# Performance work log

Hardware: AMD Instinct MI355X
Metric: run time of the kernel (lower is better)

## Reference

```python
import jax, jax.numpy as jnp
import numpy as np


def setup_inputs() -> dict:
    key = jax.random.key(0)
    ks = jax.random.split(key, 6)
    B, S, I, H = 8, 4096, 512, 512
    scale = 1.0 / np.sqrt(I)
    return {
        "x": jax.random.normal(ks[0], (B, S, I), dtype=jnp.float32),
        "h_0": jax.random.normal(ks[1], (B, H), dtype=jnp.float32),
        "W_z": jax.random.normal(ks[2], (H, I), dtype=jnp.float32) * scale,
        "b_z": jax.random.normal(ks[3], (H,), dtype=jnp.float32) * scale,
        "W_h": jax.random.normal(ks[4], (H, I), dtype=jnp.float32) * scale,
        "b_h": jax.random.normal(ks[5], (H,), dtype=jnp.float32) * scale,
    }


def reference(x, h_0, W_z, b_z, W_h, b_h):
    # Gate and candidate projections (dense GEMMs over all timesteps at once)
    z = jax.nn.sigmoid(jnp.einsum("bsi,hi->bsh", x, W_z) + b_z)  # [B,S,H]
    h_tilde = jnp.einsum("bsi,hi->bsh", x, W_h) + b_h            # [B,S,H]

    # Linear recurrence h_t = a_t * h_{t-1} + b_t with a = 1-z, b = z*h_tilde.
    # Parallel associative scan over time; h_0 folded in as element 0 (a=1, b=h_0).
    a = jnp.concatenate([jnp.ones_like(h_0)[:, None, :], 1.0 - z], axis=1)     # [B,S+1,H]
    b = jnp.concatenate([h_0[:, None, :], z * h_tilde], axis=1)                # [B,S+1,H]

    def combine(c1, c2):
        a1, b1 = c1
        a2, b2 = c2
        return a1 * a2, a2 * b1 + b2

    _, h = jax.lax.associative_scan(combine, (a, b), axis=1)
    return h[:, 1:, :]  # drop the h_0 slot -> [B,S,H]
```

## Files before the change

### kernel.cpp

```cpp
#include <hip/hip_runtime.h>
#include <hip/hip_bf16.h>
#include <stdint.h>


typedef __attribute__((ext_vector_type(8))) short short8;
typedef __attribute__((ext_vector_type(4))) float f32x4;

#define AS1 __attribute__((address_space(1)))
#define AS3 __attribute__((address_space(3)))

__device__ inline void gload_lds16(const void* g, void* l) {
  __builtin_amdgcn_global_load_lds((AS1 uint32_t*)(g), (AS3 uint32_t*)(l), 16, 0, 0);
}

__device__ inline ushort f2bf(float f) {
  union { __hip_bfloat16 h; ushort u; } v;
  v.h = __float2bfloat16(f);
  return v.u;
}

__global__ void cvt_all(const float* __restrict__ x,
                        const float* __restrict__ wz,
                        const float* __restrict__ wh,
                        ushort* __restrict__ xb,
                        ushort* __restrict__ wzb,
                        ushort* __restrict__ whb) {
  int i = blockIdx.x * 256 + threadIdx.x;
  for (; i < 4325376; i += 2048 * 256) {
    const float* s; ushort* d; int j;
    if (i < 4194304)      { s = x;  d = xb;  j = i; }
    else if (i < 4259840) { s = wz; d = wzb; j = i - 4194304; }
    else                  { s = wh; d = whb; j = i - 4259840; }
    float4 v = reinterpret_cast<const float4*>(s)[j];
    ushort4 o = make_ushort4(f2bf(v.x), f2bf(v.y), f2bf(v.z), f2bf(v.w));
    reinterpret_cast<ushort4*>(d)[j] = o;
  }
}

__global__ __launch_bounds__(256) void gemm_gate(
    const ushort* __restrict__ xb,
    const ushort* __restrict__ wzb,
    const ushort* __restrict__ whb,
    const float* __restrict__ b_z,
    const float* __restrict__ b_h,
    uint* __restrict__ ab,
    float2* __restrict__ ABc)
{
  __shared__ __align__(16) char smem[65536];

  const int t  = threadIdx.x;
  const int w  = t >> 6;
  const int l  = t & 63;
  const int lm = l & 15;
  const int lk = l >> 4;
  const int wm = w >> 1, wn = w & 1;
  const int bx = blockIdx.x;
  const int m0 = bx * 128;
  const int n0 = blockIdx.y * 64;

  const int srow = t >> 2;
  const int ssl  = t & 3;

  f32x4 accz[4][2], acch[4][2];
  #pragma unroll
  for (int m = 0; m < 4; ++m)
    #pragma unroll
    for (int n = 0; n < 2; ++n) {
      accz[m][n] = (f32x4){0.f, 0.f, 0.f, 0.f};
      acch[m][n] = (f32x4){0.f, 0.f, 0.f, 0.f};
    }

  auto stage = [&](int sel, int kt) {
    char* base = smem + sel * 16384;
    const int k0 = kt * 32;
    #pragma unroll
    for (int j = 0; j < 2; ++j) {
      int row = j * 64 + srow;
      int gs  = ssl ^ ((row >> 1) & 3);
      gload_lds16(xb + (size_t)(m0 + row) * 512 + k0 + gs * 8,
                  base + j * 4096 + w * 1024);
    }
    {
      int row = srow;
      int gs  = ssl ^ ((row >> 1) & 3);
      gload_lds16(wzb + (size_t)(n0 + row) * 512 + k0 + gs * 8,
                  base + 8192 + w * 1024);
      gload_lds16(whb + (size_t)(n0 + row) * 512 + k0 + gs * 8,
                  base + 12288 + w * 1024);
    }
  };

  stage(0, 0);
  stage(1, 1);
  stage(2, 2);

  #pragma unroll
  for (int kt = 0; kt < 16; ++kt) {
    const int sel = kt & 3;
    if (kt < 13) {
      stage((kt + 3) & 3, kt + 3);
      asm volatile("s_waitcnt vmcnt(12)" ::: "memory");
    } else if (kt == 13) {
      asm volatile("s_waitcnt vmcnt(8)" ::: "memory");
    } else if (kt == 14) {
      asm volatile("s_waitcnt vmcnt(4)" ::: "memory");
    } else {
      asm volatile("s_waitcnt vmcnt(0)" ::: "memory");
    }
    __builtin_amdgcn_s_barrier();

    const char* base = smem + sel * 16384;
    short8 af[4], bfz[2], bfh[2];
    #pragma unroll
    for (int m = 0; m < 4; ++m) {
      int row = wm * 64 + m * 16 + lm;
      af[m] = *(const short8*)(base + row * 64 + ((lk ^ ((row >> 1) & 3)) << 4));
    }
    #pragma unroll
    for (int n = 0; n < 2; ++n) {
      int row = wn * 32 + n * 16 + lm;
      int so  = ((lk ^ ((row >> 1) & 3)) << 4);
      bfz[n] = *(const short8*)(base + 8192  + row * 64 + so);
      bfh[n] = *(const short8*)(base + 12288 + row * 64 + so);
    }
    __builtin_amdgcn_s_setprio(1);
    #pragma unroll
    for (int m = 0; m < 4; ++m)
      #pragma unroll
      for (int n = 0; n < 2; ++n) {
        accz[m][n] = __builtin_amdgcn_mfma_f32_16x16x32_bf16(af[m], bfz[n], accz[m][n], 0, 0, 0);
        acch[m][n] = __builtin_amdgcn_mfma_f32_16x16x32_bf16(af[m], bfh[n], acch[m][n], 0, 0, 0);
      }
    __builtin_amdgcn_s_setprio(0);
    __builtin_amdgcn_s_barrier();
  }

  float bzv[2], bhv[2];
  #pragma unroll
  for (int n = 0; n < 2; ++n) {
    int col = n0 + wn * 32 + n * 16 + lm;
    bzv[n] = b_z[col];
    bhv[n] = b_h[col];
  }

  float av[4][4][2], bv[4][4][2];
  #pragma unroll
  for (int m = 0; m < 4; ++m) {
    #pragma unroll
    for (int j = 0; j < 4; ++j) {
      size_t grow = (size_t)(m0 + wm * 64 + m * 16 + lk * 4 + j);
      uint* po = ab + grow * 512 + n0 + wn * 32 + lm;
      #pragma unroll
      for (int n = 0; n < 2; ++n) {
        float uz = accz[m][n][j] + bzv[n];
        float uh = acch[m][n][j] + bhv[n];
        float z  = 1.f / (1.f + __expf(-uz));
        float a  = 1.f - z;
        float bb = z * uh;
        av[m][j][n] = a;
        bv[m][j][n] = bb;
        po[n * 16] = (uint)f2bf(a) | ((uint)f2bf(bb) << 16);
      }
    }
  }

  #pragma unroll
  for (int cb = 0; cb < 2; ++cb) {
    #pragma unroll
    for (int n = 0; n < 2; ++n) {
      float At[2], Bt[2];
      #pragma unroll
      for (int mm = 0; mm < 2; ++mm) {
        float A = 1.f, Bv = 0.f;
        #pragma unroll
        for (int j = 0; j < 4; ++j) {
          float a = av[2 * cb + mm][j][n];
          float b = bv[2 * cb + mm][j][n];
          A  = a * A;
          Bv = a * Bv + b;
        }
        float Ag = 1.f, Bg = 0.f;
        #pragma unroll
        for (int q = 0; q < 4; ++q) {
          float Aq = __shfl(A,  lm + 16 * q);
          float Bq = __shfl(Bv, lm + 16 * q);
          Ag = Aq * Ag;
          Bg = Aq * Bg + Bq;
        }
        At[mm] = Ag;
        Bt[mm] = Bg;
      }
      float Achunk = At[1] * At[0];
      float Bchunk = At[1] * Bt[0] + Bt[1];
      if (lk == 0) {
        int bidx = bx >> 5;
        int c    = (bx & 31) * 4 + wm * 2 + cb;
        int col  = n0 + wn * 32 + n * 16 + lm;
        ABc[((size_t)bidx * 512 + col) * 128 + c] = make_float2(Achunk, Bchunk);
      }
    }
  }
}

__global__ __launch_bounds__(256) void chunk_scan(
    const float2* __restrict__ ABc,
    const float* __restrict__ h0,
    float* __restrict__ Hinit)
{
  __shared__ float sm[128][4];
  const int w = threadIdx.x >> 6, l = threadIdx.x & 63;
  const int b   = blockIdx.x >> 7;
  const int h0g = (blockIdx.x & 127) * 4;
  const int h   = h0g + w;

  const float2* base = ABc + ((size_t)b * 512 + h) * 128;
  float2 s1 = base[l];
  float2 s2 = base[64 + l];

  float A1 = s1.x, B1 = s1.y;
  #pragma unroll
  for (int d = 1; d < 64; d <<= 1) {
    float uA = __shfl_up(A1, d);
    float uB = __shfl_up(B1, d);
    if (l >= d) { B1 = A1 * uB + B1; A1 = A1 * uA; }
  }
  float A2 = s2.x, B2 = s2.y;
  #pragma unroll
  for (int d = 1; d < 64; d <<= 1) {
    float uA = __shfl_up(A2, d);
    float uB = __shfl_up(B2, d);
    if (l >= d) { B2 = A2 * uB + B2; A2 = A2 * uA; }
  }
  float PA = __shfl(A1, 63), PB = __shfl(B1, 63);
  float FA = A2 * PA;
  float FB = A2 * PB + B2;

  float e1A = __shfl_up(A1, 1), e1B = __shfl_up(B1, 1);
  if (l == 0) { e1A = 1.f; e1B = 0.f; }
  float e2A = __shfl_up(FA, 1), e2B = __shfl_up(FB, 1);
  if (l == 0) { e2A = PA; e2B = PB; }

  float h0v = h0[b * 512 + h];
  sm[l][w]      = e1A * h0v + e1B;
  sm[64 + l][w] = e2A * h0v + e2B;
  __syncthreads();

  const int tt = threadIdx.x;
  if (tt < 128) {
    float4 v = *(const float4*)sm[tt];
    *(float4*)(Hinit + ((size_t)b * 128 + tt) * 512 + h0g) = v;
  }
}

__global__ __launch_bounds__(256) void scan_write(
    const uint* __restrict__ ab,
    const float* __restrict__ Hinit,
    float* __restrict__ out)
{
  int tid = blockIdx.x * 256 + threadIdx.x;
  int cg = tid & 127;
  int c  = (tid >> 7) & 127;
  int b  = tid >> 14;
  const uint4* p = reinterpret_cast<const uint4*>(ab + ((size_t)(b * 4096 + c * 32)) * 512) + cg;
  float4 hv = *reinterpret_cast<const float4*>(Hinit + ((size_t)b * 128 + c) * 512 + cg * 4);
  float4* po = reinterpret_cast<float4*>(out + ((size_t)(b * 4096 + c * 32)) * 512) + cg;
  #pragma unroll 4
  for (int t = 0; t < 32; ++t) {
    uint4 u = p[(size_t)t * 128];
    hv.x = __uint_as_float(u.x << 16) * hv.x + __uint_as_float(u.x & 0xffff0000u);
    hv.y = __uint_as_float(u.y << 16) * hv.y + __uint_as_float(u.y & 0xffff0000u);
    hv.z = __uint_as_float(u.z << 16) * hv.z + __uint_as_float(u.z & 0xffff0000u);
    hv.w = __uint_as_float(u.w << 16) * hv.w + __uint_as_float(u.w & 0xffff0000u);
    po[(size_t)t * 128] = hv;
  }
}

extern "C" void kernel_launch(void* const* d_in, const int* in_sizes, int n_in,
                              void* d_out, int out_size, void* d_ws, size_t ws_size,
                              hipStream_t stream) {
  const float* x   = (const float*)d_in[0];
  const float* h0  = (const float*)d_in[1];
  const float* W_z = (const float*)d_in[2];
  const float* b_z = (const float*)d_in[3];
  const float* W_h = (const float*)d_in[4];
  const float* b_h = (const float*)d_in[5];
  float* out = (float*)d_out;

  char* ws = (char*)d_ws;
  ushort* xb    = (ushort*)(ws);
  ushort* wzb   = (ushort*)(ws + 33554432);
  ushort* whb   = (ushort*)(ws + 34078720);
  uint*   ab    = (uint*)  (ws + 34603008);
  float2* ABc   = (float2*)(ws + 101711872);
  float*  Hinit = (float*) (ws + 105906176);

  cvt_all<<<2048, 256, 0, stream>>>(x, W_z, W_h, xb, wzb, whb);
  gemm_gate<<<dim3(256, 8), 256, 0, stream>>>(xb, wzb, whb, b_z, b_h, ab, ABc);
  chunk_scan<<<1024, 256, 0, stream>>>(ABc, h0, Hinit);
  scan_write<<<512, 256, 0, stream>>>(ab, Hinit, out);
}
```

Baseline: 98.15 us.

## Widen GEMM N-tile to 128, use triple buffering, and swizzle block order

```diff
diff --git a/kernel.cpp b/kernel.cpp
--- a/kernel.cpp
+++ b/kernel.cpp
@@ -37,7 +37,7 @@
   }
 }
 
-__global__ __launch_bounds__(256) void gemm_gate(
+__global__ __launch_bounds__(256, 2) void gemm_gate(
     const ushort* __restrict__ xb,
     const ushort* __restrict__ wzb,
     const ushort* __restrict__ whb,
@@ -46,7 +46,7 @@
     uint* __restrict__ ab,
     float2* __restrict__ ABc)
 {
-  __shared__ __align__(16) char smem[65536];
+  __shared__ __align__(16) char smem[73728];
 
   const int t  = threadIdx.x;
   const int w  = t >> 6;
@@ -54,24 +54,27 @@
   const int lm = l & 15;
   const int lk = l >> 4;
   const int wm = w >> 1, wn = w & 1;
-  const int bx = blockIdx.x;
+  const int bid  = blockIdx.x;
+  const int tile = (bid & 7) * 128 + (bid >> 3);
+  const int bx = tile >> 2;
+  const int by = tile & 3;
   const int m0 = bx * 128;
-  const int n0 = blockIdx.y * 64;
+  const int n0 = by * 128;
 
   const int srow = t >> 2;
   const int ssl  = t & 3;
 
-  f32x4 accz[4][2], acch[4][2];
-  #pragma unroll
-  for (int m = 0; m < 4; ++m)
-    #pragma unroll
-    for (int n = 0; n < 2; ++n) {
-      accz[m][n] = (f32x4){0.f, 0.f, 0.f, 0.f};
-      acch[m][n] = (f32x4){0.f, 0.f, 0.f, 0.f};
-    }
+  f32x4 acc[2][4][4];
+  #pragma unroll
+  for (int q = 0; q < 2; ++q)
+    #pragma unroll
+    for (int m = 0; m < 4; ++m)
+      #pragma unroll
+      for (int n = 0; n < 4; ++n)
+        acc[q][m][n] = (f32x4){0.f, 0.f, 0.f, 0.f};
 
   auto stage = [&](int sel, int kt) {
-    char* base = smem + sel * 16384;
+    char* base = smem + sel * 24576;
     const int k0 = kt * 32;
     #pragma unroll
     for (int j = 0; j < 2; ++j) {
@@ -79,103 +82,87 @@
       int gs  = ssl ^ ((row >> 1) & 3);
       gload_lds16(xb + (size_t)(m0 + row) * 512 + k0 + gs * 8,
                   base + j * 4096 + w * 1024);
-    }
-    {
-      int row = srow;
-      int gs  = ssl ^ ((row >> 1) & 3);
       gload_lds16(wzb + (size_t)(n0 + row) * 512 + k0 + gs * 8,
-                  base + 8192 + w * 1024);
+                  base + 8192 + j * 4096 + w * 1024);
       gload_lds16(whb + (size_t)(n0 + row) * 512 + k0 + gs * 8,
-                  base + 12288 + w * 1024);
+                  base + 16384 + j * 4096 + w * 1024);
     }
   };
 
   stage(0, 0);
   stage(1, 1);
-  stage(2, 2);
 
   #pragma unroll
   for (int kt = 0; kt < 16; ++kt) {
-    const int sel = kt & 3;
-    if (kt < 13) {
-      stage((kt + 3) & 3, kt + 3);
+    const int sel = kt % 3;
+    if (kt < 14) {
+      stage((kt + 2) % 3, kt + 2);
       asm volatile("s_waitcnt vmcnt(12)" ::: "memory");
-    } else if (kt == 13) {
-      asm volatile("s_waitcnt vmcnt(8)" ::: "memory");
     } else if (kt == 14) {
-      asm volatile("s_waitcnt vmcnt(4)" ::: "memory");
+      asm volatile("s_waitcnt vmcnt(6)" ::: "memory");
     } else {
       asm volatile("s_waitcnt vmcnt(0)" ::: "memory");
     }
     __builtin_amdgcn_s_barrier();
 
-    const char* base = smem + sel * 16384;
-    short8 af[4], bfz[2], bfh[2];
+    const char* base = smem + sel * 24576;
+    short8 af[4], bfz[4], bfh[4];
     #pragma unroll
     for (int m = 0; m < 4; ++m) {
       int row = wm * 64 + m * 16 + lm;
       af[m] = *(const short8*)(base + row * 64 + ((lk ^ ((row >> 1) & 3)) << 4));
     }
     #pragma unroll
-    for (int n = 0; n < 2; ++n) {
-      int row = wn * 32 + n * 16 + lm;
+    for (int n = 0; n < 4; ++n) {
+      int row = wn * 64 + n * 16 + lm;
       int so  = ((lk ^ ((row >> 1) & 3)) << 4);
       bfz[n] = *(const short8*)(base + 8192  + row * 64 + so);
-      bfh[n] = *(const short8*)(base + 12288 + row * 64 + so);
+      bfh[n] = *(const short8*)(base + 16384 + row * 64 + so);
     }
     __builtin_amdgcn_s_setprio(1);
     #pragma unroll
     for (int m = 0; m < 4; ++m)
       #pragma unroll
-      for (int n = 0; n < 2; ++n) {
-        accz[m][n] = __builtin_amdgcn_mfma_f32_16x16x32_bf16(af[m], bfz[n], accz[m][n], 0, 0, 0);
-        acch[m][n] = __builtin_amdgcn_mfma_f32_16x16x32_bf16(af[m], bfh[n], acch[m][n], 0, 0, 0);
+      for (int n = 0; n < 4; ++n) {
+        acc[0][m][n] = __builtin_amdgcn_mfma_f32_16x16x32_bf16(af[m], bfz[n], acc[0][m][n], 0, 0, 0);
+        acc[1][m][n] = __builtin_amdgcn_mfma_f32_16x16x32_bf16(af[m], bfh[n], acc[1][m][n], 0, 0, 0);
       }
     __builtin_amdgcn_s_setprio(0);
     __builtin_amdgcn_s_barrier();
   }
 
-  float bzv[2], bhv[2];
-  #pragma unroll
-  for (int n = 0; n < 2; ++n) {
-    int col = n0 + wn * 32 + n * 16 + lm;
-    bzv[n] = b_z[col];
-    bhv[n] = b_h[col];
-  }
-
-  float av[4][4][2], bv[4][4][2];
-  #pragma unroll
-  for (int m = 0; m < 4; ++m) {
-    #pragma unroll
-    for (int j = 0; j < 4; ++j) {
-      size_t grow = (size_t)(m0 + wm * 64 + m * 16 + lk * 4 + j);
-      uint* po = ab + grow * 512 + n0 + wn * 32 + lm;
-      #pragma unroll
-      for (int n = 0; n < 2; ++n) {
-        float uz = accz[m][n][j] + bzv[n];
-        float uh = acch[m][n][j] + bhv[n];
+  #pragma unroll
+  for (int n = 0; n < 4; ++n) {
+    const int col = n0 + wn * 64 + n * 16 + lm;
+    const float bzn = b_z[col];
+    const float bhn = b_h[col];
+    float av[4][4], bv[4][4];
+    #pragma unroll
+    for (int m = 0; m < 4; ++m) {
+      #pragma unroll
+      for (int j = 0; j < 4; ++j) {
+        size_t grow = (size_t)(m0 + wm * 64 + m * 16 + lk * 4 + j);
+        float uz = acc[0][m][n][j] + bzn;
+        float uh = acc[1][m][n][j] + bhn;
         float z  = 1.f / (1.f + __expf(-uz));
         float a  = 1.f - z;
         float bb = z * uh;
-        av[m][j][n] = a;
-        bv[m][j][n] = bb;
-        po[n * 16] = (uint)f2bf(a) | ((uint)f2bf(bb) << 16);
-      }
-    }
-  }
-
-  #pragma unroll
-  for (int cb = 0; cb < 2; ++cb) {
-    #pragma unroll
-    for (int n = 0; n < 2; ++n) {
+        av[m][j] = a;
+        bv[m][j] = bb;
+        ab[grow * 512 + n0 + wn * 64 + n * 16 + lm] =
+            (uint)f2bf(a) | ((uint)f2bf(bb) << 16);
+      }
+    }
+    #pragma unroll
+    for (int cb = 0; cb < 2; ++cb) {
       float At[2], Bt[2];
       #pragma unroll
       for (int mm = 0; mm < 2; ++mm) {
         float A = 1.f, Bv = 0.f;
         #pragma unroll
         for (int j = 0; j < 4; ++j) {
-          float a = av[2 * cb + mm][j][n];
-          float b = bv[2 * cb + mm][j][n];
+          float a = av[2 * cb + mm][j];
+          float b = bv[2 * cb + mm][j];
           A  = a * A;
           Bv = a * Bv + b;
         }
@@ -195,7 +182,6 @@
       if (lk == 0) {
         int bidx = bx >> 5;
         int c    = (bx & 31) * 4 + wm * 2 + cb;
-        int col  = n0 + wn * 32 + n * 16 + lm;
         ABc[((size_t)bidx * 512 + col) * 128 + c] = make_float2(Achunk, Bchunk);
       }
     }
@@ -295,7 +281,7 @@
   float*  Hinit = (float*) (ws + 105906176);
 
   cvt_all<<<2048, 256, 0, stream>>>(x, W_z, W_h, xb, wzb, whb);
-  gemm_gate<<<dim3(256, 8), 256, 0, stream>>>(xb, wzb, whb, b_z, b_h, ab, ABc);
+  gemm_gate<<<1024, 256, 0, stream>>>(xb, wzb, whb, b_z, b_h, ab, ABc);
   chunk_scan<<<1024, 256, 0, stream>>>(ABc, h0, Hinit);
   scan_write<<<512, 256, 0, stream>>>(ab, Hinit, out);
 }
```

Result: faster. 94.55 us (-3.7%).
